# Kernel tuning notes

Hardware: AMD Instinct MI355X
Metric: run time of the kernel (lower is better)

## Reference

```python
import jax, jax.numpy as jnp
import numpy as np

EPS = 1e-5

def _conv1d(x, w, b, stride=2):
    # x: [N, Cin, L], w: [Cout, Cin, K]
    y = jax.lax.conv_general_dilated(x, w, (stride,), [(1, 1)],
                                     dimension_numbers=('NCH', 'OIH', 'NCH'))
    return y + b[None, :, None]

def _bn_train(x, g, b):
    # BatchNorm1d in training mode, normalized over the batch axis (axis=1 of [T,B,F])
    m = x.mean(axis=1, keepdims=True)
    v = x.var(axis=1, keepdims=True)  # biased variance, as torch uses for normalization
    return (x - m) * jax.lax.rsqrt(v + EPS) * g + b

def setup_inputs() -> dict:
    key = jax.random.key(0)
    ks = jax.random.split(key, 20)
    T, B, C, L, F = 128, 64, 4, 2048, 64
    H = 45  # conv hidden/out channels
    d = {
        'signals': jax.random.normal(ks[0], (T, B, C, L), jnp.float32),
        'feats':   jax.random.normal(ks[1], (T, B, F), jnp.float32),
    }
    # CNN1d: depth=5 conv layers, k=3, stride=2, pad=1
    def he(k, shape, fan_in):
        return jax.random.normal(k, shape, jnp.float32) * np.float32(np.sqrt(2.0 / fan_in))
    d['conv_w0'] = he(ks[2], (H, C, 3), C * 3); d['conv_b0'] = jnp.zeros((H,), jnp.float32)
    d['conv_w1'] = he(ks[3], (H, H, 3), H * 3); d['conv_b1'] = jnp.zeros((H,), jnp.float32)
    d['conv_w2'] = he(ks[4], (H, H, 3), H * 3); d['conv_b2'] = jnp.zeros((H,), jnp.float32)
    d['conv_w3'] = he(ks[5], (H, H, 3), H * 3); d['conv_b3'] = jnp.zeros((H,), jnp.float32)
    d['conv_w4'] = he(ks[6], (H, H, 3), H * 3); d['conv_b4'] = jnp.zeros((H,), jnp.float32)
    # feat_encoder: BN(F) + Linear(F,5)
    d['bn1_g'] = jnp.ones((F,), jnp.float32); d['bn1_b'] = jnp.zeros((F,), jnp.float32)
    d['fe_w'] = he(ks[7], (5, F), F); d['fe_b'] = jnp.zeros((5,), jnp.float32)
    # combiner: Linear(50,10) + BN(10) + SiLU
    d['comb_w'] = he(ks[8], (10, 50), 50); d['comb_b'] = jnp.zeros((10,), jnp.float32)
    d['bn2_g'] = jnp.ones((10,), jnp.float32); d['bn2_b'] = jnp.zeros((10,), jnp.float32)
    # LSTM(input=10, hidden=3, proj_size=1): gates order i,f,g,o
    s = np.float32(1.0 / np.sqrt(3.0))
    d['w_ih'] = jax.random.uniform(ks[9], (12, 10), jnp.float32, -s, s)
    d['w_hh'] = jax.random.uniform(ks[10], (12, 1), jnp.float32, -s, s)
    d['b_ih'] = jax.random.uniform(ks[11], (12,), jnp.float32, -s, s)
    d['b_hh'] = jax.random.uniform(ks[12], (12,), jnp.float32, -s, s)
    d['w_hr'] = jax.random.uniform(ks[13], (1, 3), jnp.float32, -s, s)
    return d

def reference(signals, feats,
              conv_w0, conv_b0, conv_w1, conv_b1, conv_w2, conv_b2,
              conv_w3, conv_b3, conv_w4, conv_b4,
              bn1_g, bn1_b, fe_w, fe_b,
              comb_w, comb_b, bn2_g, bn2_b,
              w_ih, w_hh, b_ih, b_hh, w_hr):
    T, B, C, L = signals.shape
    # --- ConvEncoder, batched over all T*B samples (CNN1d has no batch-dependent stats) ---
    x = signals.reshape(T * B, C, L)
    for w, b in ((conv_w0, conv_b0), (conv_w1, conv_b1), (conv_w2, conv_b2),
                 (conv_w3, conv_b3), (conv_w4, conv_b4)):
        x = jax.nn.relu(_conv1d(x, w, b, stride=2))
    conved = x.mean(axis=-1).reshape(T, B, -1)  # [T, B, 45]
    # --- feat encoder: per-timestep BatchNorm (batch stats over B) + Linear ---
    fe = _bn_train(feats, bn1_g, bn1_b)
    fe = jnp.einsum('tbf,of->tbo', fe, fe_w) + fe_b  # [T, B, 5]
    # --- combiner: Linear + per-timestep BN + SiLU ---
    both = jnp.concatenate([conved, fe], axis=-1)  # [T, B, 50]
    z = jnp.einsum('tbf,of->tbo', both, comb_w) + comb_b  # [T, B, 10]
    z = jax.nn.silu(_bn_train(z, bn2_g, bn2_b))
    # --- LSTM(10, 3, proj_size=1) ---
    def step(carry, x_t):
        h, c = carry  # h: [B,1], c: [B,3]
        gates = x_t @ w_ih.T + b_ih + h @ w_hh.T + b_hh  # [B,12]
        i, f, g, o = jnp.split(gates, 4, axis=-1)
        c = jax.nn.sigmoid(f) * c + jax.nn.sigmoid(i) * jnp.tanh(g)
        h = (jax.nn.sigmoid(o) * jnp.tanh(c)) @ w_hr.T  # project to [B,1]
        return (h, c), h
    h0 = jnp.zeros((B, 1), z.dtype)
    c0 = jnp.zeros((B, 3), z.dtype)
    _, out = jax.lax.scan(step, (h0, c0), z)  # [T, B, 1]
    return out[..., 0]  # squeeze -> [T, B]
```

## Files before the change

kernel.cpp:

```cpp
#include <hip/hip_runtime.h>

typedef unsigned short ushort_t;
typedef unsigned int uint_t;

typedef short short8 __attribute__((ext_vector_type(8)));
typedef __bf16 bf16x8 __attribute__((ext_vector_type(8)));
typedef float fx4 __attribute__((ext_vector_type(4)));
typedef float fx16 __attribute__((ext_vector_type(16)));

__device__ __forceinline__ float bf2f(ushort_t u) {
    return __uint_as_float(((uint_t)u) << 16);
}
__device__ __forceinline__ ushort_t f2bf(float f) {
    uint_t x = __float_as_uint(f);
    return (ushort_t)((x + 0x7fffu + ((x >> 16) & 1u)) >> 16);
}
__device__ __forceinline__ uint_t pkbf(float lo, float hi) {
    return (uint_t)f2bf(lo) | ((uint_t)f2bf(hi) << 16);
}
__device__ __forceinline__ float ldx(const void* p, long i, int mode) {
    return mode ? bf2f(((const ushort_t*)p)[i]) : ((const float*)p)[i];
}

#define OFF_WF   0
#define OFF_W1F  18432
#define OFF_BIAS 19200
#define OFF_MODE 19456
#define OFF_PART 19520
#define OFF_Z    412736

#define INROWS 258
#define O_IN   0
#define O_L1   4128
#define O_L2   20640
#define O_L3   28960
#define L_TOTAL 61856
#define O_L4   O_L1
#define O_SUM  O_L2

__device__ __forceinline__ int swz(int r, int blk) {
    return (r << 7) + ((blk ^ ((r >> 1) & 7)) << 4);
}
__device__ __forceinline__ fx4 mfma16(fx4 acc, short8 a, short8 b) {
    return __builtin_amdgcn_mfma_f32_16x16x32_bf16(
        __builtin_bit_cast(bf16x8, a), __builtin_bit_cast(bf16x8, b), acc, 0, 0, 0);
}
__device__ __forceinline__ fx16 mfma32(fx16 acc, short8 a, short8 b) {
    return __builtin_amdgcn_mfma_f32_32x32x16_bf16(
        __builtin_bit_cast(bf16x8, a), __builtin_bit_cast(bf16x8, b), acc, 0, 0, 0);
}
__device__ __forceinline__ fx16 zero16() {
    fx16 z;
    #pragma unroll
    for (int i = 0; i < 16; i++) z[i] = 0.f;
    return z;
}
__device__ __forceinline__ fx16 bias16(const float* bp, int chf, int h) {
    fx16 r;
    #pragma unroll
    for (int q = 0; q < 4; q++) {
        fx4 b4 = *(const fx4*)(bp + 32 * chf + 8 * q + 4 * h);
        r[4 * q + 0] = b4.x; r[4 * q + 1] = b4.y;
        r[4 * q + 2] = b4.z; r[4 * q + 3] = b4.w;
    }
    return r;
}
__device__ __forceinline__ void store32(char* base, int r, int chf, int h, fx16 acc) {
    const int off = h << 3;
    const int nq = chf ? 2 : 4;
    #pragma unroll
    for (int q = 0; q < 4; q++) {
        if (q < nq) {
            uint2 p;
            p.x = pkbf(fmaxf(acc[4 * q + 0], 0.f), fmaxf(acc[4 * q + 1], 0.f));
            p.y = pkbf(fmaxf(acc[4 * q + 2], 0.f), fmaxf(acc[4 * q + 3], 0.f));
            *(uint2*)(base + swz(r, q + 4 * chf) + off) = p;
        }
    }
}

__global__ __launch_bounds__(256) void prep_kernel(
    const void* sig, const void* w0, const void* b0, const void* w1, const void* b1,
    const void* w2, const void* b2, const void* w3, const void* b3,
    const void* w4, const void* b4, float* wt, int* mode_out)
{
    __shared__ int cnt[4];
    __shared__ int smode;
    const int tid = threadIdx.x;
    {
        const uint_t* su = (const uint_t*)sig;
        int local = 0;
        for (int i = tid; i < 4096; i += 256) {
            uint_t e = (su[i] >> 7) & 0xFFu;
            local += (e >= 112u && e <= 144u) ? 1 : 0;
        }
        for (int off = 32; off > 0; off >>= 1) local += __shfl_down(local, off, 64);
        if ((tid & 63) == 0) cnt[tid >> 6] = local;
        __syncthreads();
        if (tid == 0) {
            int t = cnt[0] + cnt[1] + cnt[2] + cnt[3];
            int m = (t >= 2048) ? 1 : 0;
            smode = m;
            *mode_out = m;
        }
        __syncthreads();
    }
    const int mode = smode;

    ushort_t* wfu = (ushort_t*)wt;
    const void* wsrc[4] = {w1, w2, w3, w4};
    for (int idx = tid; idx < 36864; idx += 256) {
        int j = idx & 7, l = (idx >> 3) & 63;
        int F = idx >> 9;
        int m = F % 3, kk = (F / 3) % 3, chf = (F / 9) & 1, layer = F / 18;
        int co = 32 * chf + (l & 31);
        int ci = 16 * m + 8 * (l >> 5) + j;
        float v = (co < 45 && ci < 45) ? ldx(wsrc[layer], co * 135 + ci * 3 + kk, mode) : 0.f;
        wfu[idx] = f2bf(v);
    }
    ushort_t* w1u = (ushort_t*)(wt + OFF_W1F);
    for (int idx = tid; idx < 1536; idx += 256) {
        int j = idx & 7, l = (idx >> 3) & 63, ct = idx >> 9;
        int g = l >> 4, co = 16 * ct + (l & 15);
        float v = (co < 45 && g < 3 && j < 4) ? ldx(w0, co * 12 + j * 3 + g, mode) : 0.f;
        w1u[idx] = f2bf(v);
    }
    float* bias = wt + OFF_BIAS;
    const void* bsrc[5] = {b0, b1, b2, b3, b4};
    for (int idx = tid; idx < 240; idx += 256) {
        int l = idx / 48, co = idx % 48;
        bias[idx] = (co < 45) ? ldx(bsrc[l], co, mode) : 0.f;
    }
}

__global__ __launch_bounds__(256, 2) void conv_kernel(
    const void* sig, const float* wt, const int* mode_p, float* partial)
{
    __shared__ __align__(16) char lds[L_TOTAL];
    const int tid  = threadIdx.x;
    const int lane = tid & 63;
    const int w    = __builtin_amdgcn_readfirstlane(tid >> 6);
    const int s    = blockIdx.x;
    const int mode = *mode_p;
    const long sbase = (long)s * 8192;

    const short8* wf   = (const short8*)wt;
    const short8* w1f  = (const short8*)(wt + OFF_W1F);
    const float*  bias = wt + OFF_BIAS;

    const int h   = lane >> 5;
    const int l31 = lane & 31;
    const int l15 = lane & 15;
    const int g   = lane >> 4;
    const int chf = w & 1;

    short8 a1[3], aL2[9], aL3[9];
    #pragma unroll
    for (int ct = 0; ct < 3; ct++) a1[ct] = w1f[ct * 64 + lane];
    #pragma unroll
    for (int f = 0; f < 9; f++) aL2[f] = wf[(chf * 9 + f) * 64 + lane];
    {
        const int c3 = (w < 2) ? w : chf;
        #pragma unroll
        for (int f = 0; f < 9; f++) aL3[f] = wf[((2 + c3) * 9 + f) * 64 + lane];
    }
    fx4 b1v[3];
    #pragma unroll
    for (int ct = 0; ct < 3; ct++) b1v[ct] = *(const fx4*)(bias + 16 * ct + 4 * g);

    char* inb = lds + O_IN;
    char* l1b = lds + O_L1;
    char* l2b = lds + O_L2;
    char* l3b = lds + O_L3;

    {
        for (int ri = tid; ri < INROWS; ri += 256) {
            int x = ri - 1;
            uint_t p0 = 0, p1 = 0;
            if (x >= 0 && x < 2048) {
                float f0 = ldx(sig, sbase + x, mode);
                float f1 = ldx(sig, sbase + 2048 + x, mode);
                float f2 = ldx(sig, sbase + 4096 + x, mode);
                float f3 = ldx(sig, sbase + 6144 + x, mode);
                p0 = pkbf(f0, f1); p1 = pkbf(f2, f3);
            }
            uint4 vv; vv.x = p0; vv.y = p1; vv.z = 0; vv.w = 0;
            *(uint4*)(inb + ri * 16) = vv;
        }
        if (tid < 32) {
            *(uint_t*)(l1b + tid * 4) = 0;
            *(uint_t*)(l2b + tid * 4) = 0;
            *(uint_t*)(l3b + tid * 4) = 0;
        }
    }
    __syncthreads();

    for (int k = 0; k < 8; k++) {
        if (k > 0 && tid < 32)
            *(uint_t*)(l2b + tid * 4) = *(const uint_t*)(l2b + 64 * 128 + tid * 4);
        #pragma unroll
        for (int u = 0; u < 2; u++) {
            const int cl = (w + 4 * u) * 16 + l15;
            short8 bfrag = *(const short8*)(inb + (2 * cl + g) * 16);
            fx4 c0 = mfma16(b1v[0], a1[0], bfrag);
            fx4 c1 = mfma16(b1v[1], a1[1], bfrag);
            fx4 c2 = mfma16(b1v[2], a1[2], bfrag);
            const int r = 1 + cl;
            const int off = (g & 1) << 3;
            const int bq = g >> 1;
            uint2 p;
            p.x = pkbf(fmaxf(c0.x, 0.f), fmaxf(c0.y, 0.f));
            p.y = pkbf(fmaxf(c0.z, 0.f), fmaxf(c0.w, 0.f));
            *(uint2*)(l1b + swz(r, 0 + bq) + off) = p;
            p.x = pkbf(fmaxf(c1.x, 0.f), fmaxf(c1.y, 0.f));
            p.y = pkbf(fmaxf(c1.z, 0.f), fmaxf(c1.w, 0.f));
            *(uint2*)(l1b + swz(r, 2 + bq) + off) = p;
            p.x = pkbf(fmaxf(c2.x, 0.f), fmaxf(c2.y, 0.f));
            p.y = pkbf(fmaxf(c2.z, 0.f), fmaxf(c2.w, 0.f));
            *(uint2*)(l1b + swz(r, 4 + bq) + off) = p;
        }
        __syncthreads();

        {
            const int cl = (w >> 1) * 32 + l31;
            const int rb = 2 * cl;
            fx16 s0 = bias16(bias + 48, chf, h);
            fx16 s1 = zero16(), s2 = zero16();
            #pragma unroll
            for (int m = 0; m < 3; m++) {
                short8 bA = *(const short8*)(l1b + swz(rb + 0, 2 * m + h));
                short8 bB = *(const short8*)(l1b + swz(rb + 1, 2 * m + h));
                short8 bC = *(const short8*)(l1b + swz(rb + 2, 2 * m + h));
                s0 = mfma32(s0, aL2[0 + m], bA);
                s1 = mfma32(s1, aL2[3 + m], bB);
                s2 = mfma32(s2, aL2[6 + m], bC);
            }
            fx16 acc = s0 + s1 + s2;
            store32(l2b, 1 + cl, chf, h, acc);
        }
        __syncthreads();

        if (w < 2) {
            const int cl = l31;
            const int rb = 2 * cl;
            fx16 s0 = bias16(bias + 96, w, h);
            fx16 s1 = zero16(), s2 = zero16();
            #pragma unroll
            for (int m = 0; m < 3; m++) {
                short8 bA = *(const short8*)(l2b + swz(rb + 0, 2 * m + h));
                short8 bB = *(const short8*)(l2b + swz(rb + 1, 2 * m + h));
                short8 bC = *(const short8*)(l2b + swz(rb + 2, 2 * m + h));
                s0 = mfma32(s0, aL3[0 + m], bA);
                s1 = mfma32(s1, aL3[3 + m], bB);
                s2 = mfma32(s2, aL3[6 + m], bC);
            }
            fx16 acc = s0 + s1 + s2;
            store32(l3b, 1 + 32 * k + cl, w, h, acc);
            if (tid < 32)
                *(uint_t*)(l1b + tid * 4) = *(const uint_t*)(l1b + 128 * 128 + tid * 4);
        } else if (k < 7) {
            const int base_x = 256 * (k + 1) - 1;
            for (int ri = tid - 128; ri < INROWS; ri += 128) {
                int x = base_x + ri;
                uint_t p0 = 0, p1 = 0;
                if (x < 2048) {
                    float f0 = ldx(sig, sbase + x, mode);
                    float f1 = ldx(sig, sbase + 2048 + x, mode);
                    float f2 = ldx(sig, sbase + 4096 + x, mode);
                    float f3 = ldx(sig, sbase + 6144 + x, mode);
                    p0 = pkbf(f0, f1); p1 = pkbf(f2, f3);
                }
                uint4 vv; vv.x = p0; vv.y = p1; vv.z = 0; vv.w = 0;
                *(uint4*)(inb + ri * 16) = vv;
            }
        }
        __syncthreads();
    }

    {
        short8 a4[9];
        #pragma unroll
        for (int f = 0; f < 9; f++) a4[f] = wf[((4 + chf) * 9 + f) * 64 + lane];
        char* l4b = lds + O_L4;
        if (tid < 32) *(uint_t*)(l4b + tid * 4) = 0;
        #pragma unroll
        for (int u = 0; u < 2; u++) {
            const int ct = (w >> 1) + 2 * u;
            const int cl = ct * 32 + l31;
            const int rb = 2 * cl;
            fx16 s0 = bias16(bias + 144, chf, h);
            fx16 s1 = zero16(), s2 = zero16();
            #pragma unroll
            for (int m = 0; m < 3; m++) {
                short8 bA = *(const short8*)(l3b + swz(rb + 0, 2 * m + h));
                short8 bB = *(const short8*)(l3b + swz(rb + 1, 2 * m + h));
                short8 bC = *(const short8*)(l3b + swz(rb + 2, 2 * m + h));
                s0 = mfma32(s0, a4[0 + m], bA);
                s1 = mfma32(s1, a4[3 + m], bB);
                s2 = mfma32(s2, a4[6 + m], bC);
            }
            fx16 acc = s0 + s1 + s2;
            store32(l4b, 1 + cl, chf, h, acc);
        }
    }
    __syncthreads();

    {
        short8 a5[9];
        #pragma unroll
        for (int f = 0; f < 9; f++) a5[f] = wf[((6 + chf) * 9 + f) * 64 + lane];
        const char* l4b = lds + O_L4;
        float* sums = (float*)(lds + O_SUM);
        const int ct = w >> 1;
        const int cl = ct * 32 + l31;
        const int rb = 2 * cl;
        fx16 s0 = bias16(bias + 192, chf, h);
        fx16 s1 = zero16(), s2 = zero16();
        #pragma unroll
        for (int m = 0; m < 3; m++) {
            short8 bA = *(const short8*)(l4b + swz(rb + 0, 2 * m + h));
            short8 bB = *(const short8*)(l4b + swz(rb + 1, 2 * m + h));
            short8 bC = *(const short8*)(l4b + swz(rb + 2, 2 * m + h));
            s0 = mfma32(s0, a5[0 + m], bA);
            s1 = mfma32(s1, a5[3 + m], bB);
            s2 = mfma32(s2, a5[6 + m], bC);
        }
        fx16 acc = s0 + s1 + s2;
        #pragma unroll
        for (int i = 0; i < 16; i++) {
            float v = fmaxf(acc[i], 0.f);
            v += __shfl_xor(v, 1, 64);
            v += __shfl_xor(v, 2, 64);
            v += __shfl_xor(v, 4, 64);
            v += __shfl_xor(v, 8, 64);
            v += __shfl_xor(v, 16, 64);
            acc[i] = v;
        }
        if (l31 == 0) {
            #pragma unroll
            for (int i = 0; i < 16; i++) {
                int co = 32 * chf + 8 * (i >> 2) + 4 * h + (i & 3);
                if (co < 45) sums[ct * 48 + co] = acc[i];
            }
        }
    }
    __syncthreads();
    if (tid < 45) {
        const float* sums = (const float*)(lds + O_SUM);
        partial[s * 48 + tid] = (sums[tid] + sums[48 + tid]) * (1.f / 64.f);
    }
}

__global__ __launch_bounds__(64) void combiner_kernel(
    const void* feats, const void* bn1_g, const void* bn1_b,
    const void* fe_w, const void* fe_b, const void* comb_w, const void* comb_b,
    const void* bn2_g, const void* bn2_b, const int* mode_p,
    const float* partial, float* z)
{
    __shared__ float sf[64 * 65];
    __shared__ float s1[64], bb1[64];
    __shared__ float fw[320], cw[500];
    __shared__ float zs[640];
    __shared__ float st2[10], bt2[10];
    const int t = blockIdx.x, tid = threadIdx.x;
    const int mode = *mode_p;

    for (int idx = tid; idx < 4096; idx += 64) {
        int b = idx >> 6, f = idx & 63;
        sf[b * 65 + f] = ldx(feats, (long)t * 4096 + idx, mode);
    }
    for (int idx = tid; idx < 320; idx += 64) fw[idx] = ldx(fe_w, idx, mode);
    for (int idx = tid; idx < 500; idx += 64) cw[idx] = ldx(comb_w, idx, mode);
    __syncthreads();
    {
        const int f = tid;
        float m = 0.f, q = 0.f;
        for (int b = 0; b < 64; b++) { float x = sf[b * 65 + f]; m += x; q += x * x; }
        m *= (1.f / 64.f); q = q * (1.f / 64.f) - m * m;
        float sc = ldx(bn1_g, f, mode) * rsqrtf(q + 1e-5f);
        s1[f] = sc; bb1[f] = ldx(bn1_b, f, mode) - m * sc;
    }
    __syncthreads();
    const int b = tid;
    float fe[5];
    #pragma unroll
    for (int o = 0; o < 5; o++) fe[o] = ldx(fe_b, o, mode);
    for (int f = 0; f < 64; f++) {
        float x = sf[b * 65 + f] * s1[f] + bb1[f];
        #pragma unroll
        for (int o = 0; o < 5; o++) fe[o] += x * fw[o * 64 + f];
    }
    float zv[10];
    #pragma unroll
    for (int o = 0; o < 10; o++) zv[o] = ldx(comb_b, o, mode);
    const float* ps = partial + (t * 64 + b) * 48;
    for (int co = 0; co < 45; co++) {
        float cv = ps[co];
        #pragma unroll
        for (int o = 0; o < 10; o++) zv[o] += cv * cw[o * 50 + co];
    }
    #pragma unroll
    for (int o5 = 0; o5 < 5; o5++) {
        #pragma unroll
        for (int o = 0; o < 10; o++) zv[o] += fe[o5] * cw[o * 50 + 45 + o5];
    }
    #pragma unroll
    for (int o = 0; o < 10; o++) zs[o * 64 + b] = zv[o];
    __syncthreads();
    if (tid < 10) {
        const int o = tid; float m = 0.f, q = 0.f;
        for (int bb = 0; bb < 64; bb++) { float x = zs[o * 64 + bb]; m += x; q += x * x; }
        m *= (1.f / 64.f); q = q * (1.f / 64.f) - m * m;
        float sc = ldx(bn2_g, o, mode) * rsqrtf(q + 1e-5f);
        st2[o] = sc; bt2[o] = ldx(bn2_b, o, mode) - m * sc;
    }
    __syncthreads();
    #pragma unroll
    for (int o = 0; o < 10; o++) {
        float x = zv[o] * st2[o] + bt2[o];
        z[t * 640 + b * 10 + o] = x / (1.f + __expf(-x));
    }
}

__global__ __launch_bounds__(64) void lstm_kernel(
    const void* w_ih, const void* w_hh, const void* b_ih, const void* b_hh,
    const void* w_hr, const int* mode_p, const float* z, float* out)
{
    __shared__ float wih[120], whh[12], bsum[12], whr[3];
    const int tid = threadIdx.x;
    const int mode = *mode_p;
    for (int i = tid; i < 120; i += 64) wih[i] = ldx(w_ih, i, mode);
    if (tid < 12) { whh[tid] = ldx(w_hh, tid, mode); bsum[tid] = ldx(b_ih, tid, mode) + ldx(b_hh, tid, mode); }
    if (tid < 3)  whr[tid] = ldx(w_hr, tid, mode);
    __syncthreads();

    const int b = tid;
    float h = 0.f, c[3] = {0.f, 0.f, 0.f};
    for (int t = 0; t < 128; t++) {
        float x[10];
        #pragma unroll
        for (int j = 0; j < 10; j++) x[j] = z[t * 640 + b * 10 + j];
        float g[12];
        #pragma unroll
        for (int i = 0; i < 12; i++) {
            float a = bsum[i] + whh[i] * h;
            #pragma unroll
            for (int j = 0; j < 10; j++) a += wih[i * 10 + j] * x[j];
            g[i] = a;
        }
        float hv = 0.f;
        #pragma unroll
        for (int d = 0; d < 3; d++) {
            float fi = 1.f / (1.f + __expf(-g[3 + d]));
            float ii = 1.f / (1.f + __expf(-g[d]));
            float gg = tanhf(g[6 + d]);
            c[d] = fi * c[d] + ii * gg;
            float oo = 1.f / (1.f + __expf(-g[9 + d]));
            hv += whr[d] * (oo * tanhf(c[d]));
        }
        h = hv;
        out[t * 64 + b] = h;
    }
}

extern "C" void kernel_launch(void* const* d_in, const int* in_sizes, int n_in,
                              void* d_out, int out_size, void* d_ws, size_t ws_size,
                              hipStream_t stream)
{
    const void* signals = d_in[0];
    const void* feats   = d_in[1];
    const void* cw0 = d_in[2];  const void* cb0 = d_in[3];
    const void* cw1 = d_in[4];  const void* cb1 = d_in[5];
    const void* cw2 = d_in[6];  const void* cb2 = d_in[7];
    const void* cw3 = d_in[8];  const void* cb3 = d_in[9];
    const void* cw4 = d_in[10]; const void* cb4 = d_in[11];
    const void* bn1_g = d_in[12]; const void* bn1_b = d_in[13];
    const void* fe_w  = d_in[14]; const void* fe_b  = d_in[15];
    const void* comb_w = d_in[16]; const void* comb_b = d_in[17];
    const void* bn2_g = d_in[18]; const void* bn2_b = d_in[19];
    const void* w_ih = d_in[20]; const void* w_hh = d_in[21];
    const void* b_ih = d_in[22]; const void* b_hh = d_in[23];
    const void* w_hr = d_in[24];

    float* ws      = (float*)d_ws;
    float* wt      = ws;
    int*   mode_p  = (int*)(ws + OFF_MODE);
    float* partial = ws + OFF_PART;
    float* z       = ws + OFF_Z;

    prep_kernel<<<1, 256, 0, stream>>>(signals, cw0, cb0, cw1, cb1, cw2, cb2,
                                       cw3, cb3, cw4, cb4, wt, mode_p);
    conv_kernel<<<8192, 256, 0, stream>>>(signals, wt, mode_p, partial);
    combiner_kernel<<<128, 64, 0, stream>>>(feats, bn1_g, bn1_b, fe_w, fe_b,
                                            comb_w, comb_b, bn2_g, bn2_b, mode_p, partial, z);
    lstm_kernel<<<1, 64, 0, stream>>>(w_ih, w_hh, b_ih, b_hh, w_hr, mode_p, z, (float*)d_out);
}
```

Baseline: 1.082 ms.

## Stream conv layers 4-5 through rolling LDS buffers to raise occupancy

Conv layers 4 and 5 now run inside the chunk loop with small rolling LDS buffers instead of after it, which shrinks LDS use so four blocks can fit per CU instead of two. The input staging buffer is compacted from 16 to 8 bytes per row, and layer 5 switches to 16x16 MFMA tiles with partial sums accumulated in LDS. The LSTM replaces tanhf with an exp-based tanh. This aims to hide latency through higher occupancy and less end-of-kernel serial work, at the cost of extra barrier-coupled work per chunk, register pressure under the tighter launch bound, and slightly different tanh numerics.

Measured after the change: 1.489 ms. +37.7%, slower.

```diff
diff --git a/kernel.cpp b/kernel.cpp
--- a/kernel.cpp
+++ b/kernel.cpp
@@ -24,19 +24,19 @@
 
 #define OFF_WF   0
 #define OFF_W1F  18432
-#define OFF_BIAS 19200
-#define OFF_MODE 19456
-#define OFF_PART 19520
-#define OFF_Z    412736
-
-#define INROWS 258
+#define OFF_W5F  19200
+#define OFF_BIAS 23808
+#define OFF_MODE 24064
+#define OFF_PART 24576
+#define OFF_Z    417792
+
 #define O_IN   0
-#define O_L1   4128
-#define O_L2   20640
-#define O_L3   28960
-#define L_TOTAL 61856
-#define O_L4   O_L1
-#define O_SUM  O_L2
+#define O_L1   2064
+#define O_L2   18576
+#define O_L3   26896
+#define O_L4   35216
+#define O_SUM  39440
+#define L_TOTAL 39632
 
 __device__ __forceinline__ int swz(int r, int blk) {
     return (r << 7) + ((blk ^ ((r >> 1) & 7)) << 4);
@@ -76,6 +76,49 @@
             p.y = pkbf(fmaxf(acc[4 * q + 2], 0.f), fmaxf(acc[4 * q + 3], 0.f));
             *(uint2*)(base + swz(r, q + 4 * chf) + off) = p;
         }
+    }
+}
+__device__ __forceinline__ void conv32(char* dst, int dstRow, const char* src,
+                                       const short8* wfrag, const float* bp,
+                                       int chf, int h, int lane, int l31) {
+    short8 a[9];
+    #pragma unroll
+    for (int f = 0; f < 9; f++) a[f] = wfrag[f * 64 + lane];
+    const int rb = 2 * l31;
+    fx16 s0 = bias16(bp, chf, h);
+    fx16 s1 = zero16();
+    #pragma unroll
+    for (int m = 0; m < 3; m++) {
+        short8 bA = *(const short8*)(src + swz(rb + 0, 2 * m + h));
+        short8 bB = *(const short8*)(src + swz(rb + 1, 2 * m + h));
+        short8 bC = *(const short8*)(src + swz(rb + 2, 2 * m + h));
+        s0 = mfma32(s0, a[0 + m], bA);
+        s1 = mfma32(s1, a[3 + m], bB);
+        s0 = mfma32(s0, a[6 + m], bC);
+    }
+    store32(dst, dstRow, chf, h, s0 + s1);
+}
+__device__ __forceinline__ void l5step(const char* l4b, const short8* w5f,
+                                       const float* bias, float* sums,
+                                       int ct, int g, int l15, int lane) {
+    fx4 acc = *(const fx4*)(bias + 192 + 16 * ct + 4 * g);
+    #pragma unroll
+    for (int t = 0; t < 3; t++) {
+        #pragma unroll
+        for (int m = 0; m < 2; m++) {
+            short8 a = w5f[((ct * 3 + t) * 2 + m) * 64 + lane];
+            uint4 dv = *(const uint4*)(l4b + swz(2 * l15 + t, 4 * m + g));
+            acc = mfma16(acc, a, __builtin_bit_cast(short8, dv));
+        }
+    }
+    #pragma unroll
+    for (int i = 0; i < 4; i++) {
+        float v = fmaxf(acc[i], 0.f);
+        v += __shfl_xor(v, 1, 64);
+        v += __shfl_xor(v, 2, 64);
+        v += __shfl_xor(v, 4, 64);
+        v += __shfl_xor(v, 8, 64);
+        if (l15 == 0) sums[16 * ct + 4 * g + i] += v;
     }
 }
 
@@ -125,6 +168,16 @@
         float v = (co < 45 && g < 3 && j < 4) ? ldx(w0, co * 12 + j * 3 + g, mode) : 0.f;
         w1u[idx] = f2bf(v);
     }
+    ushort_t* w5u = (ushort_t*)(wt + OFF_W5F);
+    for (int idx = tid; idx < 9216; idx += 256) {
+        int j = idx & 7, l = (idx >> 3) & 63;
+        int F = idx >> 9;
+        int m = F & 1, t = (F >> 1) % 3, ct = (F >> 1) / 3;
+        int co = 16 * ct + (l & 15);
+        int ci = 32 * m + 8 * (l >> 4) + j;
+        float v = (co < 45 && ci < 45) ? ldx(w4, co * 135 + ci * 3 + t, mode) : 0.f;
+        w5u[idx] = f2bf(v);
+    }
     float* bias = wt + OFF_BIAS;
     const void* bsrc[5] = {b0, b1, b2, b3, b4};
     for (int idx = tid; idx < 240; idx += 256) {
@@ -133,7 +186,7 @@
     }
 }
 
-__global__ __launch_bounds__(256, 2) void conv_kernel(
+__global__ __launch_bounds__(256, 4) void conv_kernel(
     const void* sig, const float* wt, const int* mode_p, float* partial)
 {
     __shared__ __align__(16) char lds[L_TOTAL];
@@ -146,6 +199,7 @@
 
     const short8* wf   = (const short8*)wt;
     const short8* w1f  = (const short8*)(wt + OFF_W1F);
+    const short8* w5f  = (const short8*)(wt + OFF_W5F);
     const float*  bias = wt + OFF_BIAS;
 
     const int h   = lane >> 5;
@@ -154,16 +208,11 @@
     const int g   = lane >> 4;
     const int chf = w & 1;
 
-    short8 a1[3], aL2[9], aL3[9];
+    short8 a1[3], aL2[9];
     #pragma unroll
     for (int ct = 0; ct < 3; ct++) a1[ct] = w1f[ct * 64 + lane];
     #pragma unroll
     for (int f = 0; f < 9; f++) aL2[f] = wf[(chf * 9 + f) * 64 + lane];
-    {
-        const int c3 = (w < 2) ? w : chf;
-        #pragma unroll
-        for (int f = 0; f < 9; f++) aL3[f] = wf[((2 + c3) * 9 + f) * 64 + lane];
-    }
     fx4 b1v[3];
     #pragma unroll
     for (int ct = 0; ct < 3; ct++) b1v[ct] = *(const fx4*)(bias + 16 * ct + 4 * g);
@@ -172,36 +221,43 @@
     char* l1b = lds + O_L1;
     char* l2b = lds + O_L2;
     char* l3b = lds + O_L3;
-
-    {
-        for (int ri = tid; ri < INROWS; ri += 256) {
-            int x = ri - 1;
-            uint_t p0 = 0, p1 = 0;
-            if (x >= 0 && x < 2048) {
-                float f0 = ldx(sig, sbase + x, mode);
-                float f1 = ldx(sig, sbase + 2048 + x, mode);
-                float f2 = ldx(sig, sbase + 4096 + x, mode);
-                float f3 = ldx(sig, sbase + 6144 + x, mode);
-                p0 = pkbf(f0, f1); p1 = pkbf(f2, f3);
-            }
-            uint4 vv; vv.x = p0; vv.y = p1; vv.z = 0; vv.w = 0;
-            *(uint4*)(inb + ri * 16) = vv;
-        }
-        if (tid < 32) {
-            *(uint_t*)(l1b + tid * 4) = 0;
-            *(uint_t*)(l2b + tid * 4) = 0;
-            *(uint_t*)(l3b + tid * 4) = 0;
-        }
-    }
-    __syncthreads();
-
-    for (int k = 0; k < 8; k++) {
-        if (k > 0 && tid < 32)
+    char* l4b = lds + O_L4;
+    float* sums = (float*)(lds + O_SUM);
+
+    for (int ri = tid; ri < 258; ri += 256) {
+        int x = ri - 1;
+        uint_t p0 = 0, p1 = 0;
+        if (x >= 0 && x < 2048) {
+            float f0 = ldx(sig, sbase + x, mode);
+            float f1 = ldx(sig, sbase + 2048 + x, mode);
+            float f2 = ldx(sig, sbase + 4096 + x, mode);
+            float f3 = ldx(sig, sbase + 6144 + x, mode);
+            p0 = pkbf(f0, f1); p1 = pkbf(f2, f3);
+        }
+        uint2 vv; vv.x = p0; vv.y = p1;
+        *(uint2*)(inb + ri * 8) = vv;
+    }
+    if (tid < 32) {
+        *(uint_t*)(l1b + tid * 4) = 0;
+        *(uint_t*)(l2b + tid * 4) = 0;
+        *(uint_t*)(l3b + tid * 4) = 0;
+    }
+    for (int i = tid; i < 1056; i += 256) ((uint_t*)l4b)[i] = 0;
+    if (tid < 48) sums[tid] = 0.f;
+    __syncthreads();
+
+    for (int c = 0; c < 8; c++) {
+        const int evenc = ((c & 1) == 0);
+        if (c > 0 && tid < 32)
             *(uint_t*)(l2b + tid * 4) = *(const uint_t*)(l2b + 64 * 128 + tid * 4);
+        if (!evenc && c >= 3 && tid < 32)
+            *(uint_t*)(l4b + tid * 4) = *(const uint_t*)(l4b + 32 * 128 + tid * 4);
         #pragma unroll
         for (int u = 0; u < 2; u++) {
             const int cl = (w + 4 * u) * 16 + l15;
-            short8 bfrag = *(const short8*)(inb + (2 * cl + g) * 16);
+            uint2 d = *(const uint2*)(inb + (2 * cl + g) * 8);
+            uint4 dz; dz.x = d.x; dz.y = d.y; dz.z = 0; dz.w = 0;
+            short8 bfrag = __builtin_bit_cast(short8, dz);
             fx4 c0 = mfma16(b1v[0], a1[0], bfrag);
             fx4 c1 = mfma16(b1v[1], a1[1], bfrag);
             fx4 c2 = mfma16(b1v[2], a1[2], bfrag);
@@ -219,13 +275,17 @@
             p.y = pkbf(fmaxf(c2.z, 0.f), fmaxf(c2.w, 0.f));
             *(uint2*)(l1b + swz(r, 4 + bq) + off) = p;
         }
+        if (evenc && c >= 2 && w < 2)
+            conv32(l4b, 1 + l31, l3b, wf + (4 + w) * 9 * 64, bias + 144, w, h, lane, l31);
         __syncthreads();
 
+        if (evenc && c >= 2 && tid < 32)
+            *(uint_t*)(l3b + tid * 4) = *(const uint_t*)(l3b + 64 * 128 + tid * 4);
         {
             const int cl = (w >> 1) * 32 + l31;
             const int rb = 2 * cl;
             fx16 s0 = bias16(bias + 48, chf, h);
-            fx16 s1 = zero16(), s2 = zero16();
+            fx16 s1 = zero16();
             #pragma unroll
             for (int m = 0; m < 3; m++) {
                 short8 bA = *(const short8*)(l1b + swz(rb + 0, 2 * m + h));
@@ -233,122 +293,57 @@
                 short8 bC = *(const short8*)(l1b + swz(rb + 2, 2 * m + h));
                 s0 = mfma32(s0, aL2[0 + m], bA);
                 s1 = mfma32(s1, aL2[3 + m], bB);
-                s2 = mfma32(s2, aL2[6 + m], bC);
+                s0 = mfma32(s0, aL2[6 + m], bC);
             }
-            fx16 acc = s0 + s1 + s2;
-            store32(l2b, 1 + cl, chf, h, acc);
+            store32(l2b, 1 + cl, chf, h, s0 + s1);
         }
         __syncthreads();
 
         if (w < 2) {
-            const int cl = l31;
-            const int rb = 2 * cl;
-            fx16 s0 = bias16(bias + 96, w, h);
-            fx16 s1 = zero16(), s2 = zero16();
-            #pragma unroll
-            for (int m = 0; m < 3; m++) {
-                short8 bA = *(const short8*)(l2b + swz(rb + 0, 2 * m + h));
-                short8 bB = *(const short8*)(l2b + swz(rb + 1, 2 * m + h));
-                short8 bC = *(const short8*)(l2b + swz(rb + 2, 2 * m + h));
-                s0 = mfma32(s0, aL3[0 + m], bA);
-                s1 = mfma32(s1, aL3[3 + m], bB);
-                s2 = mfma32(s2, aL3[6 + m], bC);
-            }
-            fx16 acc = s0 + s1 + s2;
-            store32(l3b, 1 + 32 * k + cl, w, h, acc);
+            conv32(l3b, 1 + (c & 1) * 32 + l31, l2b, wf + (2 + w) * 9 * 64,
+                   bias + 96, w, h, lane, l31);
             if (tid < 32)
                 *(uint_t*)(l1b + tid * 4) = *(const uint_t*)(l1b + 128 * 128 + tid * 4);
-        } else if (k < 7) {
-            const int base_x = 256 * (k + 1) - 1;
-            for (int ri = tid - 128; ri < INROWS; ri += 128) {
-                int x = base_x + ri;
-                uint_t p0 = 0, p1 = 0;
-                if (x < 2048) {
-                    float f0 = ldx(sig, sbase + x, mode);
-                    float f1 = ldx(sig, sbase + 2048 + x, mode);
-                    float f2 = ldx(sig, sbase + 4096 + x, mode);
-                    float f3 = ldx(sig, sbase + 6144 + x, mode);
-                    p0 = pkbf(f0, f1); p1 = pkbf(f2, f3);
+        } else {
+            if (c < 7) {
+                const int base_x = 256 * (c + 1) - 1;
+                for (int ri = tid - 128; ri < 258; ri += 128) {
+                    int x = base_x + ri;
+                    uint_t p0 = 0, p1 = 0;
+                    if (x < 2048) {
+                        float f0 = ldx(sig, sbase + x, mode);
+                        float f1 = ldx(sig, sbase + 2048 + x, mode);
+                        float f2 = ldx(sig, sbase + 4096 + x, mode);
+                        float f3 = ldx(sig, sbase + 6144 + x, mode);
+                        p0 = pkbf(f0, f1); p1 = pkbf(f2, f3);
+                    }
+                    uint2 vv; vv.x = p0; vv.y = p1;
+                    *(uint2*)(inb + ri * 8) = vv;
                 }
-                uint4 vv; vv.x = p0; vv.y = p1; vv.z = 0; vv.w = 0;
-                *(uint4*)(inb + ri * 16) = vv;
             }
+            if (evenc && c >= 2) {
+                if (w == 2) {
+                    l5step(l4b, w5f, bias, sums, 0, g, l15, lane);
+                    l5step(l4b, w5f, bias, sums, 1, g, l15, lane);
+                } else {
+                    l5step(l4b, w5f, bias, sums, 2, g, l15, lane);
+                }
+            }
         }
         __syncthreads();
     }
 
-    {
-        short8 a4[9];
-        #pragma unroll
-        for (int f = 0; f < 9; f++) a4[f] = wf[((4 + chf) * 9 + f) * 64 + lane];
-        char* l4b = lds + O_L4;
-        if (tid < 32) *(uint_t*)(l4b + tid * 4) = 0;
-        #pragma unroll
-        for (int u = 0; u < 2; u++) {
-            const int ct = (w >> 1) + 2 * u;
-            const int cl = ct * 32 + l31;
-            const int rb = 2 * cl;
-            fx16 s0 = bias16(bias + 144, chf, h);
-            fx16 s1 = zero16(), s2 = zero16();
-            #pragma unroll
-            for (int m = 0; m < 3; m++) {
-                short8 bA = *(const short8*)(l3b + swz(rb + 0, 2 * m + h));
-                short8 bB = *(const short8*)(l3b + swz(rb + 1, 2 * m + h));
-                short8 bC = *(const short8*)(l3b + swz(rb + 2, 2 * m + h));
-                s0 = mfma32(s0, a4[0 + m], bA);
-                s1 = mfma32(s1, a4[3 + m], bB);
-                s2 = mfma32(s2, a4[6 + m], bC);
-            }
-            fx16 acc = s0 + s1 + s2;
-            store32(l4b, 1 + cl, chf, h, acc);
-        }
-    }
-    __syncthreads();
-
-    {
-        short8 a5[9];
-        #pragma unroll
-        for (int f = 0; f < 9; f++) a5[f] = wf[((6 + chf) * 9 + f) * 64 + lane];
-        const char* l4b = lds + O_L4;
-        float* sums = (float*)(lds + O_SUM);
-        const int ct = w >> 1;
-        const int cl = ct * 32 + l31;
-        const int rb = 2 * cl;
-        fx16 s0 = bias16(bias + 192, chf, h);
-        fx16 s1 = zero16(), s2 = zero16();
-        #pragma unroll
-        for (int m = 0; m < 3; m++) {
-            short8 bA = *(const short8*)(l4b + swz(rb + 0, 2 * m + h));
-            short8 bB = *(const short8*)(l4b + swz(rb + 1, 2 * m + h));
-            short8 bC = *(const short8*)(l4b + swz(rb + 2, 2 * m + h));
-            s0 = mfma32(s0, a5[0 + m], bA);
-            s1 = mfma32(s1, a5[3 + m], bB);
-            s2 = mfma32(s2, a5[6 + m], bC);
-        }
-        fx16 acc = s0 + s1 + s2;
-        #pragma unroll
-        for (int i = 0; i < 16; i++) {
-            float v = fmaxf(acc[i], 0.f);
-            v += __shfl_xor(v, 1, 64);
-            v += __shfl_xor(v, 2, 64);
-            v += __shfl_xor(v, 4, 64);
-            v += __shfl_xor(v, 8, 64);
-            v += __shfl_xor(v, 16, 64);
-            acc[i] = v;
-        }
-        if (l31 == 0) {
-            #pragma unroll
-            for (int i = 0; i < 16; i++) {
-                int co = 32 * chf + 8 * (i >> 2) + 4 * h + (i & 3);
-                if (co < 45) sums[ct * 48 + co] = acc[i];
-            }
-        }
-    }
-    __syncthreads();
-    if (tid < 45) {
-        const float* sums = (const float*)(lds + O_SUM);
-        partial[s * 48 + tid] = (sums[tid] + sums[48 + tid]) * (1.f / 64.f);
-    }
+    if (w < 2)
+        conv32(l4b, 1 + l31, l3b, wf + (4 + w) * 9 * 64, bias + 144, w, h, lane, l31);
+    __syncthreads();
+    if (w == 2) {
+        l5step(l4b, w5f, bias, sums, 0, g, l15, lane);
+        l5step(l4b, w5f, bias, sums, 1, g, l15, lane);
+    } else if (w == 3) {
+        l5step(l4b, w5f, bias, sums, 2, g, l15, lane);
+    }
+    __syncthreads();
+    if (tid < 45) partial[s * 48 + tid] = sums[tid] * (1.f / 64.f);
 }
 
 __global__ __launch_bounds__(64) void combiner_kernel(
@@ -422,6 +417,10 @@
     }
 }
 
+__device__ __forceinline__ float fast_tanh(float x) {
+    float e = __expf(-2.f * x);
+    return (1.f - e) / (1.f + e);
+}
 __global__ __launch_bounds__(64) void lstm_kernel(
     const void* w_ih, const void* w_hh, const void* b_ih, const void* b_hh,
     const void* w_hr, const int* mode_p, const float* z, float* out)
@@ -453,10 +452,10 @@
         for (int d = 0; d < 3; d++) {
             float fi = 1.f / (1.f + __expf(-g[3 + d]));
             float ii = 1.f / (1.f + __expf(-g[d]));
-            float gg = tanhf(g[6 + d]);
+            float gg = fast_tanh(g[6 + d]);
             c[d] = fi * c[d] + ii * gg;
             float oo = 1.f / (1.f + __expf(-g[9 + d]));
-            hv += whr[d] * (oo * tanhf(c[d]));
+            hv += whr[d] * (oo * fast_tanh(c[d]));
         }
         h = hv;
         out[t * 64 + b] = h;
```
